# Kernel optimization log

Hardware: AMD Instinct MI355X
Metric: run time of the kernel (lower is better)

Reference implementation:

```python
import jax, jax.numpy as jnp
import numpy as np

N = 50000   # nodes
E = 800000  # edges (before self-loops)
B = 256     # graphs in batch
F = 128     # input feature dim
H = 4       # heads per layer
C = 64      # out_channels per head
NEG_SLOPE = 0.2


def setup_inputs() -> dict:
    key = jax.random.key(0)
    ks = jax.random.split(key, 16)
    s = 0.05
    inp = {
        "x": jax.random.normal(ks[0], (N, F), dtype=jnp.float32),
        "edge_index": jax.random.randint(ks[1], (2, E), 0, N, dtype=jnp.int32),
        "batch": jnp.sort(jax.random.randint(ks[2], (N,), 0, B, dtype=jnp.int32)),
        # layer 1: F -> H*C
        "W1": jax.random.normal(ks[3], (F, H * C), dtype=jnp.float32) * s,
        "as1": jax.random.normal(ks[4], (H, C), dtype=jnp.float32) * s,
        "ad1": jax.random.normal(ks[5], (H, C), dtype=jnp.float32) * s,
        "b1": jnp.zeros((H * C,), dtype=jnp.float32),
        # layer 2: H*C -> H*C
        "W2": jax.random.normal(ks[6], (H * C, H * C), dtype=jnp.float32) * s,
        "as2": jax.random.normal(ks[7], (H, C), dtype=jnp.float32) * s,
        "ad2": jax.random.normal(ks[8], (H, C), dtype=jnp.float32) * s,
        "b2": jnp.zeros((H * C,), dtype=jnp.float32),
        # layer 3: H*C -> H*C
        "W3": jax.random.normal(ks[9], (H * C, H * C), dtype=jnp.float32) * s,
        "as3": jax.random.normal(ks[10], (H, C), dtype=jnp.float32) * s,
        "ad3": jax.random.normal(ks[11], (H, C), dtype=jnp.float32) * s,
        "b3": jnp.zeros((H * C,), dtype=jnp.float32),
    }
    return inp


def _gat_layer(x, src, dst, W, a_src, a_dst, bias):
    """PyG GATConv (concat=True, self-loops already included in src/dst)."""
    n = x.shape[0]
    xh = (x @ W).reshape(n, H, C)                      # [N,H,C]
    alpha_s = jnp.sum(xh * a_src, axis=-1)             # [N,H]
    alpha_d = jnp.sum(xh * a_dst, axis=-1)             # [N,H]
    logits = alpha_s[src] + alpha_d[dst]               # [E',H]
    logits = jnp.where(logits > 0, logits, NEG_SLOPE * logits)  # LeakyReLU
    # segment-wise softmax over destination neighborhoods
    m = jax.lax.stop_gradient(jax.ops.segment_max(logits, dst, num_segments=n))
    e = jnp.exp(logits - m[dst])
    z = jax.ops.segment_sum(e, dst, num_segments=n)
    alpha = e / (z[dst] + 1e-16)                       # [E',H]
    msg = xh[src] * alpha[:, :, None]                  # [E',H,C]
    out = jax.ops.segment_sum(msg, dst, num_segments=n)  # [N,H,C]
    return out.reshape(n, H * C) + bias


def reference(x, edge_index, batch, W1, as1, ad1, b1, W2, as2, ad2, b2, W3, as3, ad3, b3):
    n = x.shape[0]
    loops = jnp.arange(n, dtype=edge_index.dtype)
    src = jnp.concatenate([edge_index[0], loops])
    dst = jnp.concatenate([edge_index[1], loops])
    # dropout is identity at inference; activation = ReLU between layers
    h = jax.nn.relu(_gat_layer(x, src, dst, W1, as1, ad1, b1))
    h = jax.nn.relu(_gat_layer(h, src, dst, W2, as2, ad2, b2))
    h = _gat_layer(h, src, dst, W3, as3, ad3, b3)
    pooled = jax.ops.segment_max(h, batch, num_segments=B)  # global max pool -> [B, H*C]
    return jnp.squeeze(pooled)
```

## Files before the change

### kernel.cpp

```cpp
#include <hip/hip_runtime.h>
#include <hip/hip_fp16.h>
#include <math.h>

#define NN 50000
#define NE 800000
#define NT 850000
#define NB 256
#define FIN 128
#define HC 256
#define NH 4
#define CD 64
#define NEG 0.2f
#define SCAN_B 196
#define PSPL 8

typedef _Float16 half8 __attribute__((ext_vector_type(8)));
typedef float f32x4 __attribute__((ext_vector_type(4)));

__device__ __forceinline__ void gld16(const void* g, void* l) {
    __builtin_amdgcn_global_load_lds(
        (const __attribute__((address_space(1))) void*)g,
        (__attribute__((address_space(3))) void*)l, 16, 0, 0);
}


__global__ void zero_int_kernel(int* __restrict__ p, int n) {
    int i = blockIdx.x * blockDim.x + threadIdx.x;
    if (i < n) p[i] = 0;
}

__global__ void hist_kernel(const int* __restrict__ ei, int* __restrict__ cnt) {
    int e = blockIdx.x * blockDim.x + threadIdx.x;
    if (e < NE) {
        atomicAdd(&cnt[ei[NE + e]], 1);
    } else if (e < NT) {
        atomicAdd(&cnt[e - NE], 1);
    }
}

__global__ __launch_bounds__(256) void part_kernel(const int* __restrict__ cnt,
                                                   int* __restrict__ part) {
    __shared__ int red[4];
    int i = blockIdx.x * 256 + threadIdx.x;
    int v = (i < NN) ? cnt[i] : 0;
#pragma unroll
    for (int off = 32; off > 0; off >>= 1) v += __shfl_down(v, off);
    if ((threadIdx.x & 63) == 0) red[threadIdx.x >> 6] = v;
    __syncthreads();
    if (threadIdx.x == 0) part[blockIdx.x] = red[0] + red[1] + red[2] + red[3];
}

__global__ __launch_bounds__(256) void offs_kernel(const int* __restrict__ part,
                                                   int* __restrict__ boff) {
    __shared__ int sh[256];
    int t = threadIdx.x;
    sh[t] = (t < SCAN_B) ? part[t] : 0;
    __syncthreads();
    for (int off = 1; off < 256; off <<= 1) {
        int add = (t >= off) ? sh[t - off] : 0;
        __syncthreads();
        sh[t] += add;
        __syncthreads();
    }
    boff[t] = (t == 0) ? 0 : sh[t - 1];
}

__global__ __launch_bounds__(256) void write_scan_kernel(const int* __restrict__ cnt,
        const int* __restrict__ boff, int* __restrict__ rowptr, int* __restrict__ cursor) {
    __shared__ int sh[256];
    int t = threadIdx.x;
    int i = blockIdx.x * 256 + t;
    int v = (i < NN) ? cnt[i] : 0;
    sh[t] = v;
    __syncthreads();
    for (int off = 1; off < 256; off <<= 1) {
        int add = (t >= off) ? sh[t - off] : 0;
        __syncthreads();
        sh[t] += add;
        __syncthreads();
    }
    int run = boff[blockIdx.x] + sh[t] - v;
    if (i < NN) { rowptr[i] = run; cursor[i] = run; }
    if (i == NN - 1) rowptr[NN] = run + v;
}

__global__ void scatter_kernel(const int* __restrict__ ei, int* __restrict__ cursor,
                               int* __restrict__ colsrc) {
    int e = blockIdx.x * blockDim.x + threadIdx.x;
    int s, d;
    if (e < NE)      { s = ei[e]; d = ei[NE + e]; }
    else if (e < NT) { s = e - NE; d = s; }
    else return;
    int pos = atomicAdd(&cursor[d], 1);
    colsrc[pos] = s;
}

__global__ void batch_bounds_kernel(const int* __restrict__ batch, int* __restrict__ bstart) {
    int i = blockIdx.x * blockDim.x + threadIdx.x;
    if (i >= NN) return;
    int b = batch[i];
    if (i == 0) {
        for (int bb = 0; bb <= b; ++bb) bstart[bb] = 0;
    } else {
        int pb = batch[i - 1];
        if (pb != b) for (int bb = pb + 1; bb <= b; ++bb) bstart[bb] = i;
    }
    if (i == NN - 1) {
        for (int bb = b + 1; bb <= NB; ++bb) bstart[bb] = NN;
    }
}


template<int K>
__global__ __launch_bounds__(256) void wprep_kernel(const float* __restrict__ W,
                                                    _Float16* __restrict__ WtS) {
    __shared__ float sm[8][257];
    const int t = threadIdx.x;
    const int b = blockIdx.x;
    const int kb = b * 8;
    const bool lo3 = (kb >= 2 * K);
    const int kphys = lo3 ? kb - 2 * K : (kb >= K ? kb - K : kb);
#pragma unroll
    for (int i = 0; i < 8; ++i) {
        int idx = i * 256 + t;
        sm[idx >> 8][idx & 255] = W[(size_t)(kphys + (idx >> 8)) * HC + (idx & 255)];
    }
    __syncthreads();
    half8 o;
#pragma unroll
    for (int r = 0; r < 8; ++r) {
        float w = sm[r][t];
        _Float16 h = (_Float16)w;
        o[r] = lo3 ? (_Float16)(w - (float)h) : h;
    }
    *reinterpret_cast<half8*>(&WtS[((size_t)b * 256 + t) * 8]) = o;
}


template<int K, bool F32IN>
__global__ __launch_bounds__(256) void mfma_gemm_kernel(
        const _Float16* __restrict__ Xh, const _Float16* __restrict__ Xl,
        const float* __restrict__ Xf,
        const _Float16* __restrict__ WtS, __half* __restrict__ XHo,
        const float* __restrict__ as_g, const float* __restrict__ ad_g,
        float* __restrict__ aS, float* __restrict__ aD) {
    constexpr int C3 = 3 * K;
    constexpr int NSTEP = C3 / 64;
    __shared__ __align__(16) _Float16 As[2][64 * 64];
    __shared__ __align__(16) _Float16 Bs[2][64 * 256];
    const int t = threadIdx.x;
    const int lane = t & 63;
    const int wid = t >> 6;
    const int wm = wid & 1, wn = wid >> 1;
    const int r0 = blockIdx.x * 64;
    const int l15 = lane & 15;
    const int kcl = lane >> 4;
    const int srow = t >> 2;
    const int skc0 = (t & 3) * 2;
    const int arow = min(r0 + srow, NN - 1);

    f32x4 acc[2][8];
#pragma unroll
    for (int i = 0; i < 2; ++i)
#pragma unroll
        for (int j = 0; j < 8; ++j) acc[i][j] = (f32x4)0.f;

    float4 st[4];
    auto loadA = [&](int s) {
        const int ks = s * 64;
        const int sel = (ks < K) ? 0 : (ks < 2 * K) ? 1 : 2;
        const int cbase = ks - sel * K;
        if (F32IN) {
            const float* p = Xf + (size_t)arow * K + cbase + skc0 * 8;
            st[0] = *reinterpret_cast<const float4*>(p);
            st[1] = *reinterpret_cast<const float4*>(p + 4);
            st[2] = *reinterpret_cast<const float4*>(p + 8);
            st[3] = *reinterpret_cast<const float4*>(p + 12);
        } else {
            const _Float16* src = (sel == 1) ? Xl : Xh;
            const _Float16* p = src + (size_t)arow * K + cbase + skc0 * 8;
            st[0] = *reinterpret_cast<const float4*>(p);
            st[1] = *reinterpret_cast<const float4*>(p + 8);
        }
    };
    auto writeA = [&](int buf, int s) {
        _Float16* d0 = &As[buf][(skc0 * 64 + (srow ^ skc0)) * 8];
        _Float16* d1 = &As[buf][((skc0 + 1) * 64 + (srow ^ (skc0 + 1))) * 8];
        if (F32IN) {
            const int ks = s * 64;
            const int sel = (ks < K) ? 0 : (ks < 2 * K) ? 1 : 2;
            const float* f = reinterpret_cast<const float*>(st);
            half8 h0, h1;
#pragma unroll
            for (int e = 0; e < 8; ++e) {
                float v0 = f[e], v1 = f[8 + e];
                _Float16 a = (_Float16)v0, b = (_Float16)v1;
                h0[e] = (sel == 1) ? (_Float16)(v0 - (float)a) : a;
                h1[e] = (sel == 1) ? (_Float16)(v1 - (float)b) : b;
            }
            *reinterpret_cast<half8*>(d0) = h0;
            *reinterpret_cast<half8*>(d1) = h1;
        } else {
            *reinterpret_cast<float4*>(d0) = st[0];
            *reinterpret_cast<float4*>(d1) = st[1];
        }
    };
    auto issueB = [&](int s, int buf) {
        const _Float16* bsrc = WtS + (size_t)s * (64 * 256);
#pragma unroll
        for (int r = 0; r < 8; ++r)
            gld16(bsrc + ((size_t)r * 256 + t) * 8, &Bs[buf][((size_t)r * 256 + t) * 8]);
    };

    loadA(0);
    issueB(0, 0);
    writeA(0, 0);
    __syncthreads();

    for (int s = 0; s < NSTEP; ++s) {
        const int cur = s & 1, nxt = cur ^ 1;
        const bool more = (s + 1) < NSTEP;
        if (more) {
            loadA(s + 1);
            issueB(s + 1, nxt);
        }
#pragma unroll
        for (int kk = 0; kk < 2; ++kk) {
            const int kc = kk * 4 + kcl;
            half8 a0 = *reinterpret_cast<const half8*>(
                &As[cur][(kc * 64 + ((wm * 32      + l15) ^ kc)) * 8]);
            half8 a1 = *reinterpret_cast<const half8*>(
                &As[cur][(kc * 64 + ((wm * 32 + 16 + l15) ^ kc)) * 8]);
            const _Float16* bp = &Bs[cur][(kc * 256 + wn * 128 + l15) * 8];
#pragma unroll
            for (int nf = 0; nf < 8; ++nf) {
                half8 b = *reinterpret_cast<const half8*>(bp + nf * 16 * 8);
                acc[0][nf] = __builtin_amdgcn_mfma_f32_16x16x32_f16(a0, b, acc[0][nf], 0, 0, 0);
                acc[1][nf] = __builtin_amdgcn_mfma_f32_16x16x32_f16(a1, b, acc[1][nf], 0, 0, 0);
            }
        }
        if (more) {
            writeA(nxt, s + 1);
            asm volatile("s_waitcnt vmcnt(0) lgkmcnt(0)" ::: "memory");
            __builtin_amdgcn_s_barrier();
            __builtin_amdgcn_sched_barrier(0);
        }
    }

    const int rb = r0 + wm * 32 + (lane >> 4) * 4;
    const int cb = wn * 128 + l15;
    float asv[8], adv[8];
#pragma unroll
    for (int nf = 0; nf < 8; ++nf) {
        asv[nf] = as_g[cb + nf * 16];
        adv[nf] = ad_g[cb + nf * 16];
    }
#pragma unroll
    for (int mf = 0; mf < 2; ++mf)
#pragma unroll
        for (int r = 0; r < 4; ++r) {
            int row = rb + mf * 16 + r;
            float s0 = 0.f, s1 = 0.f, d0 = 0.f, d1 = 0.f;
#pragma unroll
            for (int nf = 0; nf < 4; ++nf) {
                float a = acc[mf][nf][r], b = acc[mf][nf + 4][r];
                s0 += a * asv[nf];     d0 += a * adv[nf];
                s1 += b * asv[nf + 4]; d1 += b * adv[nf + 4];
            }
#pragma unroll
            for (int off = 1; off < 16; off <<= 1) {
                s0 += __shfl_xor(s0, off); s1 += __shfl_xor(s1, off);
                d0 += __shfl_xor(d0, off); d1 += __shfl_xor(d1, off);
            }
            if (row < NN) {
                if (l15 == 0) {
                    aS[row * 4 + 2 * wn] = s0; aS[row * 4 + 2 * wn + 1] = s1;
                    aD[row * 4 + 2 * wn] = d0; aD[row * 4 + 2 * wn + 1] = d1;
                }
#pragma unroll
                for (int nf = 0; nf < 8; ++nf)
                    XHo[(size_t)row * HC + cb + nf * 16] = __float2half(acc[mf][nf][r]);
            }
        }
}


#define LEAKY(v) ((v) > 0.f ? (v) : NEG * (v))

template<int RELU, int SPLIT>
__global__ __launch_bounds__(256) void aggregate_kernel(
        const int* __restrict__ rowptr, const int* __restrict__ colsrc,
        const float* __restrict__ aS, const float* __restrict__ aD,
        const __half* __restrict__ XH,
        const float* __restrict__ bias, float* __restrict__ OUT,
        __half* __restrict__ OUTh, __half* __restrict__ OUTl) {
    __shared__ float4 wbuf[4][64];
    __shared__ int    ibuf[4][64];
    const int wslot = threadIdx.x >> 6;
    int n = blockIdx.x * 4 + wslot;
    int lane = threadIdx.x & 63;
    bool lo = lane < 32;
    const __half2* xbase = reinterpret_cast<const __half2*>(XH);
    float4 adv = *reinterpret_cast<const float4*>(aD + n * 4);
    float zl = 0.f, zh = 0.f;
    float al0 = 0.f, al1 = 0.f, ah0 = 0.f, ah1 = 0.f;
    int jb = rowptr[n], je = rowptr[n + 1];
    for (int c0 = jb; c0 < je; c0 += 64) {
        int cnt = min(64, je - c0);
        {
            int e = min(c0 + lane, je - 1);
            int s = colsrc[e];
            float4 sv = *reinterpret_cast<const float4*>(aS + s * 4);
            float4 w;
            w.x = __expf(LEAKY(sv.x + adv.x));
            w.y = __expf(LEAKY(sv.y + adv.y));
            w.z = __expf(LEAKY(sv.z + adv.z));
            w.w = __expf(LEAKY(sv.w + adv.w));
            wbuf[wslot][lane] = w;
            ibuf[wslot][lane] = s;
        }
        int u = 0;
        for (; u + 8 <= cnt; u += 8) {
            int sidx[8];
            float4 w[8];
#pragma unroll
            for (int k = 0; k < 8; ++k) { sidx[k] = ibuf[wslot][u + k]; w[k] = wbuf[wslot][u + k]; }
            __half2 p[8], q[8];
#pragma unroll
            for (int k = 0; k < 8; ++k) {
                const __half2* xp = xbase + (size_t)sidx[k] * (HC / 2) + lane;
                p[k] = xp[0];
                q[k] = xp[64];
            }
#pragma unroll
            for (int k = 0; k < 8; ++k) {
                float wl = lo ? w[k].x : w[k].y, wh = lo ? w[k].z : w[k].w;
                float2 f = __half22float2(p[k]);
                al0 += wl * f.x; al1 += wl * f.y;
                f = __half22float2(q[k]);
                ah0 += wh * f.x; ah1 += wh * f.y;
                zl += wl; zh += wh;
            }
        }
        for (; u < cnt; ++u) {
            int s0 = ibuf[wslot][u];
            float4 w0 = wbuf[wslot][u];
            const __half2* xp = xbase + (size_t)s0 * (HC / 2) + lane;
            __half2 p0 = xp[0], q0 = xp[64];
            float w0l = lo ? w0.x : w0.y, w0h = lo ? w0.z : w0.w;
            float2 f = __half22float2(p0);
            al0 += w0l * f.x; al1 += w0l * f.y;
            f = __half22float2(q0);
            ah0 += w0h * f.x; ah1 += w0h * f.y;
            zl += w0l; zh += w0h;
        }
    }
    float izl = 1.f / (zl + 1e-16f), izh = 1.f / (zh + 1e-16f);
    float2 bl = reinterpret_cast<const float2*>(bias)[lane];
    float2 bh = reinterpret_cast<const float2*>(bias + 128)[lane];
    float o0 = al0 * izl + bl.x;
    float o1 = al1 * izl + bl.y;
    float o2 = ah0 * izh + bh.x;
    float o3 = ah1 * izh + bh.y;
    if (RELU) {
        o0 = fmaxf(o0, 0.f); o1 = fmaxf(o1, 0.f);
        o2 = fmaxf(o2, 0.f); o3 = fmaxf(o3, 0.f);
    }
    if (SPLIT) {
        __half h0 = __float2half(o0), h1 = __float2half(o1);
        __half h2 = __float2half(o2), h3 = __float2half(o3);
        __half2* ph = reinterpret_cast<__half2*>(OUTh + (size_t)n * HC) + lane;
        ph[0]  = __half2(h0, h1);
        ph[64] = __half2(h2, h3);
        __half2* pl = reinterpret_cast<__half2*>(OUTl + (size_t)n * HC) + lane;
        pl[0]  = __half2(__float2half(o0 - __half2float(h0)), __float2half(o1 - __half2float(h1)));
        pl[64] = __half2(__float2half(o2 - __half2float(h2)), __float2half(o3 - __half2float(h3)));
    } else {
        float2* op = reinterpret_cast<float2*>(OUT + (size_t)n * HC) + lane;
        op[0]  = make_float2(o0, o1);
        op[64] = make_float2(o2, o3);
    }
}


__global__ __launch_bounds__(256) void pool1_kernel(const float* __restrict__ Hf,
        const int* __restrict__ bstart, float* __restrict__ part) {
    int b = blockIdx.x / PSPL, sp = blockIdx.x % PSPL;
    int c = threadIdx.x;
    int i0 = bstart[b], i1 = bstart[b + 1];
    float m = -INFINITY;
    for (int i = i0 + sp; i < i1; i += PSPL) m = fmaxf(m, Hf[(size_t)i * HC + c]);
    part[(size_t)blockIdx.x * HC + c] = m;
}

__global__ __launch_bounds__(256) void pool2_kernel(const float* __restrict__ part,
        float* __restrict__ out) {
    int b = blockIdx.x;
    int c = threadIdx.x;
    float m = -INFINITY;
#pragma unroll
    for (int sp = 0; sp < PSPL; ++sp)
        m = fmaxf(m, part[(size_t)(b * PSPL + sp) * HC + c]);
    out[b * HC + c] = m;
}


extern "C" void kernel_launch(void* const* d_in, const int* in_sizes, int n_in,
                              void* d_out, int out_size, void* d_ws, size_t ws_size,
                              hipStream_t stream) {
    const float* x     = (const float*)d_in[0];
    const int*   ei    = (const int*)d_in[1];
    const int*   batch = (const int*)d_in[2];
    const float* W1  = (const float*)d_in[3];
    const float* as1 = (const float*)d_in[4];
    const float* ad1 = (const float*)d_in[5];
    const float* b1  = (const float*)d_in[6];
    const float* W2  = (const float*)d_in[7];
    const float* as2 = (const float*)d_in[8];
    const float* ad2 = (const float*)d_in[9];
    const float* b2  = (const float*)d_in[10];
    const float* W3  = (const float*)d_in[11];
    const float* as3 = (const float*)d_in[12];
    const float* ad3 = (const float*)d_in[13];
    const float* b3  = (const float*)d_in[14];
    float* out = (float*)d_out;

    __half* Hh  = (__half*)d_ws;
    __half* Hl  = Hh + (size_t)NN * HC;
    __half* XHh = Hl + (size_t)NN * HC;
    float* bufB = (float*)Hh;
    _Float16* WtS = (_Float16*)(XHh + (size_t)NN * HC);
    float*  aS  = (float*)(WtS + 768 * 256);
    float*  aD  = aS + NN * NH;
    float*  ppart = aD + NN * NH;
    int* cnt    = (int*)(ppart + (size_t)NB * PSPL * HC);
    int* rowptr = cnt + NN;
    int* cursor = rowptr + (NN + 1);
    int* colsrc = cursor + NN;
    int* bstart = colsrc + NT;
    int* part   = bstart + (NB + 1);
    int* boff   = part + SCAN_B;

    zero_int_kernel<<<(NN + 255) / 256, 256, 0, stream>>>(cnt, NN);
    hist_kernel<<<(NT + 255) / 256, 256, 0, stream>>>(ei, cnt);
    part_kernel<<<SCAN_B, 256, 0, stream>>>(cnt, part);
    offs_kernel<<<1, 256, 0, stream>>>(part, boff);
    write_scan_kernel<<<SCAN_B, 256, 0, stream>>>(cnt, boff, rowptr, cursor);
    scatter_kernel<<<(NT + 255) / 256, 256, 0, stream>>>(ei, cursor, colsrc);
    batch_bounds_kernel<<<(NN + 255) / 256, 256, 0, stream>>>(batch, bstart);

    const int gemm_grid = (NN + 63) / 64;
    const int node_grid = NN / 4;

    wprep_kernel<FIN><<<3 * FIN / 8, 256, 0, stream>>>(W1, WtS);
    mfma_gemm_kernel<FIN, true><<<gemm_grid, 256, 0, stream>>>(
        nullptr, nullptr, x, WtS, XHh, as1, ad1, aS, aD);
    aggregate_kernel<1, 1><<<node_grid, 256, 0, stream>>>(rowptr, colsrc, aS, aD, XHh, b1,
                                                          nullptr, Hh, Hl);

    wprep_kernel<HC><<<3 * HC / 8, 256, 0, stream>>>(W2, WtS);
    mfma_gemm_kernel<HC, false><<<gemm_grid, 256, 0, stream>>>(
        (_Float16*)Hh, (_Float16*)Hl, nullptr, WtS, XHh, as2, ad2, aS, aD);
    aggregate_kernel<1, 1><<<node_grid, 256, 0, stream>>>(rowptr, colsrc, aS, aD, XHh, b2,
                                                          nullptr, Hh, Hl);

    wprep_kernel<HC><<<3 * HC / 8, 256, 0, stream>>>(W3, WtS);
    mfma_gemm_kernel<HC, false><<<gemm_grid, 256, 0, stream>>>(
        (_Float16*)Hh, (_Float16*)Hl, nullptr, WtS, XHh, as3, ad3, aS, aD);
    aggregate_kernel<0, 0><<<node_grid, 256, 0, stream>>>(rowptr, colsrc, aS, aD, XHh, b3,
                                                          bufB, nullptr, nullptr);

    pool1_kernel<<<NB * PSPL, 256, 0, stream>>>(bufB, bstart, ppart);
    pool2_kernel<<<NB, 256, 0, stream>>>(ppart, out);
}
```

Before: 471.2 us.

## Use 4-stage async LDS pipeline in MFMA GEMM with pre-split fp16 input

Restructures the MFMA GEMM main loop into a 4-buffer, K=32-per-step pipeline in which both A and B tiles are loaded straight into LDS with global_load_lds. Partial vmcnt waits keep three stages in flight, and s_setprio raises priority around the MFMA burst. To make the A path uniform, the layer-1 fp32 input is pre-split into fp16 hi/lo arrays by a new split_x kernel, which removes the in-kernel conversion path. This trades an extra pass over x and more barriers per K for better overlap of memory and compute.

```diff
diff --git a/kernel.cpp b/kernel.cpp
--- a/kernel.cpp
+++ b/kernel.cpp
@@ -15,6 +15,7 @@
 #define PSPL 8
 
 typedef _Float16 half8 __attribute__((ext_vector_type(8)));
+typedef _Float16 half4v __attribute__((ext_vector_type(4)));
 typedef float f32x4 __attribute__((ext_vector_type(4)));
 
 __device__ __forceinline__ void gld16(const void* g, void* l) {
@@ -111,6 +112,22 @@
 }
 
 
+__global__ __launch_bounds__(256) void split_x_kernel(const float* __restrict__ X,
+        _Float16* __restrict__ Xh, _Float16* __restrict__ Xl) {
+    int i = blockIdx.x * 256 + threadIdx.x;
+    if (i >= NN * FIN / 4) return;
+    float4 v = reinterpret_cast<const float4*>(X)[i];
+    half4v h, l;
+    h[0] = (_Float16)v.x; h[1] = (_Float16)v.y; h[2] = (_Float16)v.z; h[3] = (_Float16)v.w;
+    l[0] = (_Float16)(v.x - (float)h[0]);
+    l[1] = (_Float16)(v.y - (float)h[1]);
+    l[2] = (_Float16)(v.z - (float)h[2]);
+    l[3] = (_Float16)(v.w - (float)h[3]);
+    reinterpret_cast<half4v*>(Xh)[i] = h;
+    reinterpret_cast<half4v*>(Xl)[i] = l;
+}
+
+
 template<int K>
 __global__ __launch_bounds__(256) void wprep_kernel(const float* __restrict__ W,
                                                     _Float16* __restrict__ WtS) {
@@ -137,17 +154,17 @@
 }
 
 
-template<int K, bool F32IN>
+template<int K>
 __global__ __launch_bounds__(256) void mfma_gemm_kernel(
         const _Float16* __restrict__ Xh, const _Float16* __restrict__ Xl,
-        const float* __restrict__ Xf,
         const _Float16* __restrict__ WtS, __half* __restrict__ XHo,
         const float* __restrict__ as_g, const float* __restrict__ ad_g,
         float* __restrict__ aS, float* __restrict__ aD) {
     constexpr int C3 = 3 * K;
-    constexpr int NSTEP = C3 / 64;
-    __shared__ __align__(16) _Float16 As[2][64 * 64];
-    __shared__ __align__(16) _Float16 Bs[2][64 * 256];
+    constexpr int NSTEP = C3 / 32;
+    constexpr int SPP = K / 32;
+    __shared__ __align__(16) _Float16 As[4][64 * 32];
+    __shared__ __align__(16) _Float16 Bs[4][32 * 256];
     const int t = threadIdx.x;
     const int lane = t & 63;
     const int wid = t >> 6;
@@ -155,9 +172,8 @@
     const int r0 = blockIdx.x * 64;
     const int l15 = lane & 15;
     const int kcl = lane >> 4;
-    const int srow = t >> 2;
-    const int skc0 = (t & 3) * 2;
-    const int arow = min(r0 + srow, NN - 1);
+    const int kcA = t >> 6;
+    const int arow = min(r0 + ((t & 63) ^ kcA), NN - 1);
 
     f32x4 acc[2][8];
 #pragma unroll
@@ -165,87 +181,55 @@
 #pragma unroll
         for (int j = 0; j < 8; ++j) acc[i][j] = (f32x4)0.f;
 
-    float4 st[4];
-    auto loadA = [&](int s) {
-        const int ks = s * 64;
-        const int sel = (ks < K) ? 0 : (ks < 2 * K) ? 1 : 2;
-        const int cbase = ks - sel * K;
-        if (F32IN) {
-            const float* p = Xf + (size_t)arow * K + cbase + skc0 * 8;
-            st[0] = *reinterpret_cast<const float4*>(p);
-            st[1] = *reinterpret_cast<const float4*>(p + 4);
-            st[2] = *reinterpret_cast<const float4*>(p + 8);
-            st[3] = *reinterpret_cast<const float4*>(p + 12);
-        } else {
-            const _Float16* src = (sel == 1) ? Xl : Xh;
-            const _Float16* p = src + (size_t)arow * K + cbase + skc0 * 8;
-            st[0] = *reinterpret_cast<const float4*>(p);
-            st[1] = *reinterpret_cast<const float4*>(p + 8);
+    auto issue = [&](int s) {
+        const int sel = s / SPP;
+        const int cbase = (s - sel * SPP) * 32;
+        const _Float16* srcA = (sel == 1) ? Xl : Xh;
+        const int buf = s & 3;
+        gld16(srcA + (size_t)arow * K + cbase + kcA * 8, &As[buf][t * 8]);
+        const _Float16* bsrc = WtS + (size_t)s * (32 * 256);
+#pragma unroll
+        for (int r = 0; r < 4; ++r)
+            gld16(bsrc + ((size_t)r * 256 + t) * 8, &Bs[buf][(r * 256 + t) * 8]);
+    };
+    auto mfma_step = [&](int s) {
+        const int buf = s & 3;
+        half8 a0 = *reinterpret_cast<const half8*>(
+            &As[buf][(kcl * 64 + ((wm * 32      + l15) ^ kcl)) * 8]);
+        half8 a1 = *reinterpret_cast<const half8*>(
+            &As[buf][(kcl * 64 + ((wm * 32 + 16 + l15) ^ kcl)) * 8]);
+        const _Float16* bp = &Bs[buf][(kcl * 256 + wn * 128 + l15) * 8];
+        __builtin_amdgcn_s_setprio(1);
+#pragma unroll
+        for (int nf = 0; nf < 8; ++nf) {
+            half8 b = *reinterpret_cast<const half8*>(bp + nf * 16 * 8);
+            acc[0][nf] = __builtin_amdgcn_mfma_f32_16x16x32_f16(a0, b, acc[0][nf], 0, 0, 0);
+            acc[1][nf] = __builtin_amdgcn_mfma_f32_16x16x32_f16(a1, b, acc[1][nf], 0, 0, 0);
         }
+        __builtin_amdgcn_s_setprio(0);
     };
-    auto writeA = [&](int buf, int s) {
-        _Float16* d0 = &As[buf][(skc0 * 64 + (srow ^ skc0)) * 8];
-        _Float16* d1 = &As[buf][((skc0 + 1) * 64 + (srow ^ (skc0 + 1))) * 8];
-        if (F32IN) {
-            const int ks = s * 64;
-            const int sel = (ks < K) ? 0 : (ks < 2 * K) ? 1 : 2;
-            const float* f = reinterpret_cast<const float*>(st);
-            half8 h0, h1;
-#pragma unroll
-            for (int e = 0; e < 8; ++e) {
-                float v0 = f[e], v1 = f[8 + e];
-                _Float16 a = (_Float16)v0, b = (_Float16)v1;
-                h0[e] = (sel == 1) ? (_Float16)(v0 - (float)a) : a;
-                h1[e] = (sel == 1) ? (_Float16)(v1 - (float)b) : b;
-            }
-            *reinterpret_cast<half8*>(d0) = h0;
-            *reinterpret_cast<half8*>(d1) = h1;
-        } else {
-            *reinterpret_cast<float4*>(d0) = st[0];
-            *reinterpret_cast<float4*>(d1) = st[1];
-        }
-    };
-    auto issueB = [&](int s, int buf) {
-        const _Float16* bsrc = WtS + (size_t)s * (64 * 256);
-#pragma unroll
-        for (int r = 0; r < 8; ++r)
-            gld16(bsrc + ((size_t)r * 256 + t) * 8, &Bs[buf][((size_t)r * 256 + t) * 8]);
-    };
-
-    loadA(0);
-    issueB(0, 0);
-    writeA(0, 0);
-    __syncthreads();
-
-    for (int s = 0; s < NSTEP; ++s) {
-        const int cur = s & 1, nxt = cur ^ 1;
-        const bool more = (s + 1) < NSTEP;
-        if (more) {
-            loadA(s + 1);
-            issueB(s + 1, nxt);
-        }
-#pragma unroll
-        for (int kk = 0; kk < 2; ++kk) {
-            const int kc = kk * 4 + kcl;
-            half8 a0 = *reinterpret_cast<const half8*>(
-                &As[cur][(kc * 64 + ((wm * 32      + l15) ^ kc)) * 8]);
-            half8 a1 = *reinterpret_cast<const half8*>(
-                &As[cur][(kc * 64 + ((wm * 32 + 16 + l15) ^ kc)) * 8]);
-            const _Float16* bp = &Bs[cur][(kc * 256 + wn * 128 + l15) * 8];
-#pragma unroll
-            for (int nf = 0; nf < 8; ++nf) {
-                half8 b = *reinterpret_cast<const half8*>(bp + nf * 16 * 8);
-                acc[0][nf] = __builtin_amdgcn_mfma_f32_16x16x32_f16(a0, b, acc[0][nf], 0, 0, 0);
-                acc[1][nf] = __builtin_amdgcn_mfma_f32_16x16x32_f16(a1, b, acc[1][nf], 0, 0, 0);
-            }
-        }
-        if (more) {
-            writeA(nxt, s + 1);
-            asm volatile("s_waitcnt vmcnt(0) lgkmcnt(0)" ::: "memory");
-            __builtin_amdgcn_s_barrier();
-            __builtin_amdgcn_sched_barrier(0);
-        }
-    }
+
+    issue(0); issue(1); issue(2);
+    asm volatile("s_waitcnt vmcnt(10)" ::: "memory");
+    __builtin_amdgcn_s_barrier();
+    __builtin_amdgcn_sched_barrier(0);
+
+    for (int s = 0; s < NSTEP - 3; ++s) {
+        issue(s + 3);
+        mfma_step(s);
+        asm volatile("s_waitcnt vmcnt(10) lgkmcnt(0)" ::: "memory");
+        __builtin_amdgcn_s_barrier();
+        __builtin_amdgcn_sched_barrier(0);
+    }
+    mfma_step(NSTEP - 3);
+    asm volatile("s_waitcnt vmcnt(5) lgkmcnt(0)" ::: "memory");
+    __builtin_amdgcn_s_barrier();
+    __builtin_amdgcn_sched_barrier(0);
+    mfma_step(NSTEP - 2);
+    asm volatile("s_waitcnt vmcnt(0) lgkmcnt(0)" ::: "memory");
+    __builtin_amdgcn_s_barrier();
+    __builtin_amdgcn_sched_barrier(0);
+    mfma_step(NSTEP - 1);
 
     const int rb = r0 + wm * 32 + (lane >> 4) * 4;
     const int cb = wn * 128 + l15;
@@ -428,6 +412,8 @@
     __half* Hh  = (__half*)d_ws;
     __half* Hl  = Hh + (size_t)NN * HC;
     __half* XHh = Hl + (size_t)NN * HC;
+    _Float16* Xh1 = (_Float16*)Hh;
+    _Float16* Xl1 = Xh1 + (size_t)NN * FIN;
     float* bufB = (float*)Hh;
     _Float16* WtS = (_Float16*)(XHh + (size_t)NN * HC);
     float*  aS  = (float*)(WtS + 768 * 256);
@@ -452,21 +438,23 @@
     const int gemm_grid = (NN + 63) / 64;
     const int node_grid = NN / 4;
 
+    split_x_kernel<<<(NN * FIN / 4 + 255) / 256, 256, 0, stream>>>(x, Xh1, Xl1);
+
     wprep_kernel<FIN><<<3 * FIN / 8, 256, 0, stream>>>(W1, WtS);
-    mfma_gemm_kernel<FIN, true><<<gemm_grid, 256, 0, stream>>>(
-        nullptr, nullptr, x, WtS, XHh, as1, ad1, aS, aD);
+    mfma_gemm_kernel<FIN><<<gemm_grid, 256, 0, stream>>>(
+        Xh1, Xl1, WtS, XHh, as1, ad1, aS, aD);
     aggregate_kernel<1, 1><<<node_grid, 256, 0, stream>>>(rowptr, colsrc, aS, aD, XHh, b1,
                                                           nullptr, Hh, Hl);
 
     wprep_kernel<HC><<<3 * HC / 8, 256, 0, stream>>>(W2, WtS);
-    mfma_gemm_kernel<HC, false><<<gemm_grid, 256, 0, stream>>>(
-        (_Float16*)Hh, (_Float16*)Hl, nullptr, WtS, XHh, as2, ad2, aS, aD);
+    mfma_gemm_kernel<HC><<<gemm_grid, 256, 0, stream>>>(
+        (_Float16*)Hh, (_Float16*)Hl, WtS, XHh, as2, ad2, aS, aD);
     aggregate_kernel<1, 1><<<node_grid, 256, 0, stream>>>(rowptr, colsrc, aS, aD, XHh, b2,
                                                           nullptr, Hh, Hl);
 
     wprep_kernel<HC><<<3 * HC / 8, 256, 0, stream>>>(W3, WtS);
-    mfma_gemm_kernel<HC, false><<<gemm_grid, 256, 0, stream>>>(
-        (_Float16*)Hh, (_Float16*)Hl, nullptr, WtS, XHh, as3, ad3, aS, aD);
+    mfma_gemm_kernel<HC><<<gemm_grid, 256, 0, stream>>>(
+        (_Float16*)Hh, (_Float16*)Hl, WtS, XHh, as3, ad3, aS, aD);
     aggregate_kernel<0, 0><<<node_grid, 256, 0, stream>>>(rowptr, colsrc, aS, aD, XHh, b3,
                                                           bufB, nullptr, nullptr);
 
```

Result: no change. 468.1 us (-0.7%).
